# Optimization experiments

Measured on AMD Instinct MI355X. Metric: run time of the kernel, lower is better.

Reference implementation:

```python
import jax, jax.numpy as jnp
import numpy as np

B, T, I, H = 512, 2048, 13, 13


def setup_inputs() -> dict:
    key = jax.random.key(0)
    ks = jax.random.split(key, 7)
    s_in = 1.0 / np.sqrt(H)
    return {
        "x": jax.random.normal(ks[0], (B, T, I), dtype=jnp.float32),
        "W_ih": jax.random.uniform(ks[1], (4 * H, I), jnp.float32, -s_in, s_in),
        "W_hh": jax.random.uniform(ks[2], (4 * H, H), jnp.float32, -s_in, s_in),
        "b_ih": jax.random.uniform(ks[3], (4 * H,), jnp.float32, -s_in, s_in),
        "b_hh": jax.random.uniform(ks[4], (4 * H,), jnp.float32, -s_in, s_in),
        "fc_w": jax.random.uniform(ks[5], (1, H), jnp.float32, -s_in, s_in),
        "fc_b": jax.random.uniform(ks[6], (1,), jnp.float32, -s_in, s_in),
    }


def _lstm(x, W_ih, W_hh, b_ih, b_hh):
    # Precompute input-to-gate projections for all timesteps: [B, T, 4H]
    xg = jnp.einsum("bti,gi->btg", x, W_ih) + b_ih + b_hh
    xg = jnp.swapaxes(xg, 0, 1)  # [T, B, 4H] for scan
    h0 = jnp.zeros((x.shape[0], H), x.dtype)
    c0 = jnp.zeros((x.shape[0], H), x.dtype)

    def step(carry, xg_t):
        h, c = carry
        gates = xg_t + h @ W_hh.T  # [B, 4H]
        i_g, f_g, g_g, o_g = jnp.split(gates, 4, axis=-1)  # PyTorch order i,f,g,o
        i_g = jax.nn.sigmoid(i_g)
        f_g = jax.nn.sigmoid(f_g)
        g_g = jnp.tanh(g_g)
        o_g = jax.nn.sigmoid(o_g)
        c_new = f_g * c + i_g * g_g
        h_new = o_g * jnp.tanh(c_new)
        return (h_new, c_new), h_new

    _, hs = jax.lax.scan(step, (h0, c0), xg)  # hs: [T, B, H]
    return jnp.swapaxes(hs, 0, 1)  # [B, T, H]


def reference(x, W_ih, W_hh, b_ih, b_hh, fc_w, fc_b):
    out = _lstm(x, W_ih, W_hh, b_ih, b_hh)  # [B, T, H]
    out = jnp.einsum("bth,oh->bto", out, fc_w) + fc_b  # [B, T, 1]
    return jax.nn.sigmoid(out)
```

## Files before the change

kernel.cpp:

```cpp
#include <hip/hip_runtime.h>

#define BB 512
#define TT 2048
#define CH 64
#define NCH (TT/CH)

__device__ __forceinline__ float fexp2(float x){ return __builtin_amdgcn_exp2f(x); }
__device__ __forceinline__ float frcp(float x){ return __builtin_amdgcn_rcpf(x); }

#define QB(v, ctrl) __int_as_float(__builtin_amdgcn_mov_dpp(__float_as_int(v), (ctrl), 0xF, 0xF, true))
#define RL(v, l)    __builtin_amdgcn_readlane((v), (l))

__global__ __launch_bounds__(128, 1) void k_fused(
    const float* __restrict__ x,
    const float* __restrict__ Wih,
    const float* __restrict__ Whh,
    const float* __restrict__ bih,
    const float* __restrict__ bhh,
    const float* __restrict__ fcw,
    const float* __restrict__ fcb,
    float* __restrict__ out)
{
  __shared__ float sxbuf[2][CH][64];

  const int tid  = threadIdx.x;
  const int wid  = tid >> 6;
  const int lane = tid & 63;
  const int b    = blockIdx.x;
  const float* xp = x + (size_t)b*(TT*13);

  float wxp[13]; float biasp = 0.f;
  float w[13];
  float kgm = 1.f, kga = 0.f, fcbias = 0.f;
  int   e = 0;
  float h = 0.f, c_ = 0.f;
  float hb0=0,hb1=0,hb2=0,hb3=0,hb4=0,hb5=0,hb6=0,hb7=0,hb8=0,hb9=0,hb10=0,hb11=0,hb12=0;
  float p0=0,p1=0,p2=0,p3=0,p4=0,p5=0,p6=0,p7=0;
  float* op = out + (size_t)b*TT;
  bool first = true;

#define FILL(bi_, t0_) do {                                                   \
    _Pragma("unroll 2")                                                       \
    for (int tt=0; tt<CH; tt+=4){                                             \
      const float* rp = xp + (size_t)((t0_)+tt)*13;                           \
      float a0=biasp, a1=biasp, a2=biasp, a3=biasp;                           \
      _Pragma("unroll")                                                       \
      for (int k=0;k<13;++k){                                                 \
        a0 = fmaf(wxp[k], rp[k],    a0);                                      \
        a1 = fmaf(wxp[k], rp[13+k], a1);                                      \
        a2 = fmaf(wxp[k], rp[26+k], a2);                                      \
        a3 = fmaf(wxp[k], rp[39+k], a3);                                      \
      }                                                                       \
      sxbuf[bi_][tt+0][lane] = a0;                                            \
      sxbuf[bi_][tt+1][lane] = a1;                                            \
      sxbuf[bi_][tt+2][lane] = a2;                                            \
      sxbuf[bi_][tt+3][lane] = a3;                                            \
    }                                                                         \
  } while(0)

#define CAPTURE(gv_, u_) do {                                                 \
    if ((u_)==1) p0=(gv_); else if ((u_)==2) p1=(gv_);                        \
    else if ((u_)==3) p2=(gv_); else if ((u_)==4) p3=(gv_);                   \
    else if ((u_)==5) p4=(gv_); else if ((u_)==6) p5=(gv_);                   \
    else if ((u_)==7) p6=(gv_);                                               \
    else { p7=(gv_);                                                          \
      if (!first){                                                            \
        if (lane == 52){                                                      \
          float4* o4 = (float4*)op;                                           \
          o4[0] = make_float4(p0,p1,p2,p3);                                   \
          o4[1] = make_float4(p4,p5,p6,p7);                                   \
        }                                                                     \
        op += 8;                                                              \
      }                                                                       \
      first = false;                                                          \
    }                                                                         \
  } while(0)

#define STEP(xv_, u_) do {                                                    \
    float dA = fmaf(w[0], hb0, (xv_));                                        \
    dA = fmaf(w[1], hb1, dA);                                                 \
    dA = fmaf(w[2], hb2, dA);                                                 \
    dA = fmaf(w[3], hb3, dA);                                                 \
    dA = fmaf(w[4], hb4, dA);                                                 \
    float dB = w[5]*hb5;                                                      \
    dB = fmaf(w[6], hb6, dB);                                                 \
    dB = fmaf(w[7], hb7, dB);                                                 \
    dB = fmaf(w[8], hb8, dB);                                                 \
    float dC = w[9]*hb9;                                                      \
    dC = fmaf(w[10], hb10, dC);                                               \
    dC = fmaf(w[11], hb11, dC);                                               \
    dC = fmaf(w[12], hb12, dC);                                               \
    float s  = (dB + dC) + dA;                                                \
    float r  = frcp(1.f + fexp2(s));                                          \
    float g  = fmaf(kgm, r, kga);                                             \
    CAPTURE(g, u_);                                                           \
    float ggb = QB(g, 0xAA);                                                  \
    float gfb = QB(g, 0x55);                                                  \
    float gob = QB(g, 0xFF);                                                  \
    float go2 = gob + gob;                                                    \
    c_ = fmaf(gfb, c_, g*ggb);                                                \
    float r2 = frcp(1.f + fexp2(c_));                                         \
    h = fmaf(go2, r2, -gob);                                                  \
    int hv_ = __float_as_int(h);                                              \
    hb0  = __int_as_float(RL(hv_, 0));                                        \
    hb1  = __int_as_float(RL(hv_, 4));                                        \
    hb2  = __int_as_float(RL(hv_, 8));                                        \
    hb3  = __int_as_float(RL(hv_, 12));                                       \
    hb4  = __int_as_float(RL(hv_, 16));                                       \
    hb5  = __int_as_float(RL(hv_, 20));                                       \
    hb6  = __int_as_float(RL(hv_, 24));                                       \
    hb7  = __int_as_float(RL(hv_, 28));                                       \
    hb8  = __int_as_float(RL(hv_, 32));                                       \
    hb9  = __int_as_float(RL(hv_, 36));                                       \
    hb10 = __int_as_float(RL(hv_, 40));                                       \
    hb11 = __int_as_float(RL(hv_, 44));                                       \
    hb12 = __int_as_float(RL(hv_, 48));                                       \
  } while(0)

#define CONSUME(bi_) do {                                                     \
    float rc[8], rn[8];                                                       \
    _Pragma("unroll")                                                         \
    for (int u=0;u<8;++u) rc[u] = sxbuf[bi_][u][e];                           \
    _Pragma("unroll 2")                                                       \
    for (int g=0; g<CH/8; ++g){                                               \
      const int tn = (g < CH/8-1) ? ((g+1)<<3) : 0;  \
      _Pragma("unroll")                                                       \
      for (int u=0;u<8;++u) rn[u] = sxbuf[bi_][tn+u][e];                      \
      STEP(rc[0],0); STEP(rc[1],1); STEP(rc[2],2); STEP(rc[3],3);             \
      STEP(rc[4],4); STEP(rc[5],5); STEP(rc[6],6); STEP(rc[7],7);             \
      _Pragma("unroll")                                                       \
      for (int u=0;u<8;++u) rc[u] = rn[u];                                    \
    }                                                                         \
  } while(0)

  if (wid == 1){
    const int  l     = lane;
    const bool fcrow = (l == 52);
    const int  row   = (l < 52) ? l : 0;
    const float kql  = (l >= 26 && l < 39) ? -2.8853900817779268f : -1.4426950408889634f;
    const float kx   = fcrow ? 0.f : kql;
    #pragma unroll
    for (int k=0;k<13;k++) wxp[k] = Wih[row*13+k]*kx;
    biasp = fcrow ? (-1.4426950408889634f * fcb[0])
                  : ((l < 52) ? (bih[row]+bhh[row])*kql : 0.f);
    FILL(0, 0);
  } else {
    const int  q   = lane & 3;
    const int  j   = lane >> 2;
    const int  jc  = (j < 13) ? j : 12;
    const bool fcl = (lane == 52);
    e = fcl ? 52 : q*13 + jc;
    const float kq = (q==2) ? -2.8853900817779268f : -1.4426950408889634f;
    kgm = (q==2) ? -5.7707801635558536f : 1.f;
    kga = (q==2) ?  2.8853900817779268f : 0.f;
    fcbias = -1.4426950408889634f * fcb[0];
    const float* wsrc = fcl ? fcw : (Whh + (size_t)e*13);
    #pragma unroll
    for (int k=0;k<13;k++) w[k] = wsrc[k]*kq;
  }
  __syncthreads();

  for (int c=0; c<NCH-1; ++c){
    if (wid == 1){ FILL((c+1)&1, (c+1)*CH); }
    else         { CONSUME(c&1); }
    __syncthreads();
  }

  if (wid == 0){
    CONSUME((NCH-1)&1);

    float s = fcbias;
    s = fmaf(w[0],  hb0,  s);
    s = fmaf(w[1],  hb1,  s);
    s = fmaf(w[2],  hb2,  s);
    s = fmaf(w[3],  hb3,  s);
    s = fmaf(w[4],  hb4,  s);
    s = fmaf(w[5],  hb5,  s);
    s = fmaf(w[6],  hb6,  s);
    s = fmaf(w[7],  hb7,  s);
    s = fmaf(w[8],  hb8,  s);
    s = fmaf(w[9],  hb9,  s);
    s = fmaf(w[10], hb10, s);
    s = fmaf(w[11], hb11, s);
    s = fmaf(w[12], hb12, s);
    float r = frcp(1.f + fexp2(s));
    if (lane == 52){
      float4* o4 = (float4*)op;
      o4[0] = make_float4(p0,p1,p2,p3);
      o4[1] = make_float4(p4,p5,p6,r);
    }
  }

#undef CONSUME
#undef STEP
#undef CAPTURE
#undef FILL
}

extern "C" void kernel_launch(void* const* d_in, const int* in_sizes, int n_in,
                              void* d_out, int out_size, void* d_ws, size_t ws_size,
                              hipStream_t stream)
{
  const float* x   = (const float*)d_in[0];
  const float* Wih = (const float*)d_in[1];
  const float* Whh = (const float*)d_in[2];
  const float* bih = (const float*)d_in[3];
  const float* bhh = (const float*)d_in[4];
  const float* fcw = (const float*)d_in[5];
  const float* fcb = (const float*)d_in[6];
  float* out = (float*)d_out;

  (void)d_ws; (void)ws_size;
  k_fused<<<dim3(BB), dim3(128), 0, stream>>>(x, Wih, Whh, bih, bhh, fcw, fcb, out);
}
```

Measured before the change: 365.4 us.

## Prefetch x chunks into registers and stage through shared memory for projection

The producer wave now loads the next chunk of raw x with coalesced per-lane loads into registers one chunk ahead, stages them into a shared raw buffer, then computes the input projections from shared memory. Before, every lane re-read the same x rows straight from global memory inside the projection loop. The aim is to hide global-load latency behind the consumer's recurrence and to replace redundant broadcast global loads with LDS reads. It costs extra shared memory and registers, plus a bounded redundant load of the final chunk.

```diff
diff --git a/kernel.cpp b/kernel.cpp
--- a/kernel.cpp
+++ b/kernel.cpp
@@ -11,7 +11,7 @@
 #define QB(v, ctrl) __int_as_float(__builtin_amdgcn_mov_dpp(__float_as_int(v), (ctrl), 0xF, 0xF, true))
 #define RL(v, l)    __builtin_amdgcn_readlane((v), (l))
 
-__global__ __launch_bounds__(128, 1) void k_fused(
+__global__ __launch_bounds__(128, 1) void k_fused2(
     const float* __restrict__ x,
     const float* __restrict__ Wih,
     const float* __restrict__ Whh,
@@ -22,6 +22,7 @@
     float* __restrict__ out)
 {
   __shared__ float sxbuf[2][CH][64];
+  __shared__ float xraw[2][CH*13];
 
   const int tid  = threadIdx.x;
   const int wid  = tid >> 6;
@@ -29,7 +30,7 @@
   const int b    = blockIdx.x;
   const float* xp = x + (size_t)b*(TT*13);
 
-  float wxp[13]; float biasp = 0.f;
+  float wxp[13]; float biasp = 0.f; float xr[13];
   float w[13];
   float kgm = 1.f, kga = 0.f, fcbias = 0.f;
   int   e = 0;
@@ -39,22 +40,25 @@
   float* op = out + (size_t)b*TT;
   bool first = true;
 
-#define FILL(bi_, t0_) do {                                                   \
-    _Pragma("unroll 2")                                                       \
-    for (int tt=0; tt<CH; tt+=4){                                             \
-      const float* rp = xp + (size_t)((t0_)+tt)*13;                           \
-      float a0=biasp, a1=biasp, a2=biasp, a3=biasp;                           \
+#define PLOAD(c_) do {                                                        \
+    const float* srcp_ = xp + (size_t)(c_)*(CH*13);                           \
+    _Pragma("unroll")                                                         \
+    for (int i=0;i<13;++i) xr[i] = srcp_[lane + (i<<6)];                      \
+  } while(0)
+
+#define PSTAGE(bi_) do {                                                      \
+    _Pragma("unroll")                                                         \
+    for (int i=0;i<13;++i) xraw[bi_][lane + (i<<6)] = xr[i];                  \
+  } while(0)
+
+#define PFILL(bi_) do {                                                       \
+    _Pragma("unroll 4")                                                       \
+    for (int tt=0; tt<CH; ++tt){                                              \
+      float a_ = biasp;                                                       \
       _Pragma("unroll")                                                       \
-      for (int k=0;k<13;++k){                                                 \
-        a0 = fmaf(wxp[k], rp[k],    a0);                                      \
-        a1 = fmaf(wxp[k], rp[13+k], a1);                                      \
-        a2 = fmaf(wxp[k], rp[26+k], a2);                                      \
-        a3 = fmaf(wxp[k], rp[39+k], a3);                                      \
-      }                                                                       \
-      sxbuf[bi_][tt+0][lane] = a0;                                            \
-      sxbuf[bi_][tt+1][lane] = a1;                                            \
-      sxbuf[bi_][tt+2][lane] = a2;                                            \
-      sxbuf[bi_][tt+3][lane] = a3;                                            \
+      for (int k=0;k<13;++k)                                                  \
+        a_ = fmaf(wxp[k], xraw[bi_][tt*13+k], a_);                            \
+      sxbuf[bi_][tt][lane] = a_;                                              \
     }                                                                         \
   } while(0)
 
@@ -143,7 +147,10 @@
     for (int k=0;k<13;k++) wxp[k] = Wih[row*13+k]*kx;
     biasp = fcrow ? (-1.4426950408889634f * fcb[0])
                   : ((l < 52) ? (bih[row]+bhh[row])*kql : 0.f);
-    FILL(0, 0);
+    PLOAD(0);
+    PSTAGE(0);
+    PLOAD(1);
+    PFILL(0);
   } else {
     const int  q   = lane & 3;
     const int  j   = lane >> 2;
@@ -161,8 +168,15 @@
   __syncthreads();
 
   for (int c=0; c<NCH-1; ++c){
-    if (wid == 1){ FILL((c+1)&1, (c+1)*CH); }
-    else         { CONSUME(c&1); }
+    if (wid == 1){
+      const int bi = (c+1)&1;
+      PSTAGE(bi);
+      const int c2 = (c+2 < NCH) ? (c+2) : (NCH-1);
+      PLOAD(c2);
+      PFILL(bi);
+    } else {
+      CONSUME(c&1);
+    }
     __syncthreads();
   }
 
@@ -194,7 +208,9 @@
 #undef CONSUME
 #undef STEP
 #undef CAPTURE
-#undef FILL
+#undef PFILL
+#undef PSTAGE
+#undef PLOAD
 }
 
 extern "C" void kernel_launch(void* const* d_in, const int* in_sizes, int n_in,
@@ -211,5 +227,5 @@
   float* out = (float*)d_out;
 
   (void)d_ws; (void)ws_size;
-  k_fused<<<dim3(BB), dim3(128), 0, stream>>>(x, Wih, Whh, bih, bhh, fcw, fcb, out);
+  k_fused2<<<dim3(BB), dim3(128), 0, stream>>>(x, Wih, Whh, bih, bhh, fcw, fcb, out);
 }
```

Result: faster. 353.2 us (-3.3%).
